# Kernel tuning notes

Measured on AMD Instinct MI355X. Metric: run time of the kernel, lower is better.

The kernel has to match this reference:

```python
import jax, jax.numpy as jnp
import numpy as np

N = 200000
HID = 256
HEADS = 8
HD = HID // HEADS
C = 1000  # num clusters


def setup_inputs() -> dict:
    key = jax.random.key(0)
    ks = jax.random.split(key, 8)
    s = 1.0 / np.sqrt(HID)
    return {
        "x": jax.random.normal(ks[0], (N, HID), dtype=jnp.float32),
        "cluster_assignments": jax.random.randint(ks[1], (N,), 0, C),
        "batch": jnp.zeros((N,), dtype=jnp.int64),
        "Wk": jax.random.uniform(ks[2], (HID, HID), minval=-s, maxval=s),
        "bk": jnp.zeros((HID,), dtype=jnp.float32),
        "Wv": jax.random.uniform(ks[3], (HID, HID), minval=-s, maxval=s),
        "bv": jnp.zeros((HID,), dtype=jnp.float32),
        "Wo": jax.random.uniform(ks[4], (HID, HID), minval=-s, maxval=s),
        "bo": jnp.zeros((HID,), dtype=jnp.float32),
        "pool_query": jax.random.normal(ks[5], (1, HEADS, HD), dtype=jnp.float32),
    }


def reference(x, cluster_assignments, batch, Wk, bk, Wv, bv, Wo, bo, pool_query):
    seg = cluster_assignments
    scale = HD ** -0.5
    keys = (x @ Wk.T + bk).reshape(-1, HEADS, HD)     # [N, H, D]
    values = (x @ Wv.T + bv).reshape(-1, HEADS, HD)   # [N, H, D]
    # attention scores per node/head against shared pool query
    scores = jnp.einsum('nhd,hd->nh', keys, pool_query[0]) * scale  # [N, H]
    # segment-wise (per-cluster) softmax over nodes, per head
    m = jax.ops.segment_max(scores, seg, num_segments=C)            # [C, H]
    e = jnp.exp(scores - m[seg])                                    # [N, H]
    z = jax.ops.segment_sum(e, seg, num_segments=C)                 # [C, H]
    w = e / z[seg]                                                  # [N, H]
    attended = (w[..., None] * values).reshape(-1, HID)             # [N, HID]
    # scatter_mean over clusters
    ssum = jax.ops.segment_sum(attended, seg, num_segments=C)       # [C, HID]
    cnt = jax.ops.segment_sum(jnp.ones((attended.shape[0],), attended.dtype), seg, num_segments=C)
    pooled = ssum / jnp.clip(cnt, 1.0)[:, None]                     # [C, HID]
    out = pooled @ Wo.T + bo                                        # [C, HID]
    return out[seg]                                                 # [N, HID]
```

## Files before the change

kernel.cpp:

```cpp
#include <hip/hip_runtime.h>
#include <math.h>

#define HID 256
#define HEADS 8
#define HD 32
#define C_CLUST 1000
#define SCALEQ 0.17677669529663687f
#define CAP 512

typedef float fx4 __attribute__((ext_vector_type(4)));

__global__ __launch_bounds__(256) void k_prep(const float* __restrict__ Wk,
                                              const float* __restrict__ bk,
                                              const float* __restrict__ pq,
                                              float* __restrict__ qk,
                                              float* __restrict__ cb,
                                              int* __restrict__ cur) {
  __shared__ float qv[HD];
  int h = blockIdx.x;
  int t = threadIdx.x;
  int g = h * 256 + t;
  for (int i = g; i < C_CLUST; i += 2048) cur[i] = 0;
  if (t < HD) qv[t] = pq[h * HD + t];
  __syncthreads();
  float a = 0.f;
#pragma unroll 8
  for (int d = 0; d < HD; ++d) a += Wk[(size_t)(h * HD + d) * HID + t] * qv[d];
  qk[h * HID + t] = a * SCALEQ;
  if (t == 0) {
    float s = 0.f;
    for (int d = 0; d < HD; ++d) s += bk[h * HD + d] * qv[d];
    cb[h] = s * SCALEQ;
  }
}

__global__ __launch_bounds__(256) void k_scores(const float* __restrict__ x,
                                                const int* __restrict__ seg,
                                                const float* __restrict__ qk,
                                                const float* __restrict__ cb,
                                                float* __restrict__ escr,
                                                int* __restrict__ cur,
                                                int* __restrict__ list, int N) {
  int lane = threadIdx.x & 63;
  int wid = (int)(((size_t)blockIdx.x * blockDim.x + threadIdx.x) >> 6);
  int nw = (int)(((size_t)gridDim.x * blockDim.x) >> 6);
  float4 q4[8];
#pragma unroll
  for (int h = 0; h < 8; ++h) q4[h] = *(const float4*)(qk + h * HID + 4 * lane);
  float cbv = cb[lane & 7];
  for (int n = wid; n < N; n += nw) {
    float4 xv = *(const float4*)(x + (size_t)n * HID + 4 * lane);
    float r0 = xv.x * q4[0].x + xv.y * q4[0].y + xv.z * q4[0].z + xv.w * q4[0].w;
    float r1 = xv.x * q4[1].x + xv.y * q4[1].y + xv.z * q4[1].z + xv.w * q4[1].w;
    float r2 = xv.x * q4[2].x + xv.y * q4[2].y + xv.z * q4[2].z + xv.w * q4[2].w;
    float r3 = xv.x * q4[3].x + xv.y * q4[3].y + xv.z * q4[3].z + xv.w * q4[3].w;
    float r4 = xv.x * q4[4].x + xv.y * q4[4].y + xv.z * q4[4].z + xv.w * q4[4].w;
    float r5 = xv.x * q4[5].x + xv.y * q4[5].y + xv.z * q4[5].z + xv.w * q4[5].w;
    float r6 = xv.x * q4[6].x + xv.y * q4[6].y + xv.z * q4[6].z + xv.w * q4[6].w;
    float r7 = xv.x * q4[7].x + xv.y * q4[7].y + xv.z * q4[7].z + xv.w * q4[7].w;
    r0 += __shfl_xor(r0, 1); r0 += __shfl_xor(r0, 2); r0 += __shfl_xor(r0, 4);
    r1 += __shfl_xor(r1, 1); r1 += __shfl_xor(r1, 2); r1 += __shfl_xor(r1, 4);
    r2 += __shfl_xor(r2, 1); r2 += __shfl_xor(r2, 2); r2 += __shfl_xor(r2, 4);
    r3 += __shfl_xor(r3, 1); r3 += __shfl_xor(r3, 2); r3 += __shfl_xor(r3, 4);
    r4 += __shfl_xor(r4, 1); r4 += __shfl_xor(r4, 2); r4 += __shfl_xor(r4, 4);
    r5 += __shfl_xor(r5, 1); r5 += __shfl_xor(r5, 2); r5 += __shfl_xor(r5, 4);
    r6 += __shfl_xor(r6, 1); r6 += __shfl_xor(r6, 2); r6 += __shfl_xor(r6, 4);
    r7 += __shfl_xor(r7, 1); r7 += __shfl_xor(r7, 2); r7 += __shfl_xor(r7, 4);
    int p = lane & 7;
    float v = (p < 4) ? ((p < 2) ? (p == 0 ? r0 : r1) : (p == 2 ? r2 : r3))
                      : ((p < 6) ? (p == 4 ? r4 : r5) : (p == 6 ? r6 : r7));
    v += __shfl_xor(v, 8); v += __shfl_xor(v, 16); v += __shfl_xor(v, 32);
    v += cbv;
    if (lane < 8) {
      int c = seg[n];
      escr[(size_t)n * 8 + lane] = __expf(v);
      if (lane == 0) {
        int pos = atomicAdd(&cur[c], 1);
        if (pos < CAP) list[c * CAP + pos] = n;
      }
    }
  }
}

__global__ __launch_bounds__(256) void k_pool(const float* __restrict__ x,
                                              const float* __restrict__ escr,
                                              const int* __restrict__ cur,
                                              const int* __restrict__ list,
                                              const float* __restrict__ Wv,
                                              const float* __restrict__ bv,
                                              const float* __restrict__ Wo,
                                              const float* __restrict__ bo,
                                              float* __restrict__ out) {
  __shared__ float e_lds[CAP][8];
  __shared__ float s_lds[8 * HID];
  __shared__ float red[32];
  __shared__ float p_lds[HID];
  __shared__ float orow[HID];
  int c = blockIdx.x;
  int t = threadIdx.x;
  int cnt = cur[c];
  if (cnt == 0) return;
  int cntL = (cnt < CAP) ? cnt : CAP;

  int h8 = t & 7;
  int i0 = t >> 3;
  int rq = t >> 6, cl = t & 63;
  const int* lp = list + c * CAP;

  float pz = 0.f;
  for (int i = i0; i < cntL; i += 32) {
    float ev = escr[(size_t)lp[i] * 8 + h8];
    e_lds[i][h8] = ev;
    pz += ev;
  }
  pz += __shfl_xor(pz, 8);
  pz += __shfl_xor(pz, 16);
  pz += __shfl_xor(pz, 32);
  if (cl < 8) red[rq * 8 + cl] = pz;
  __syncthreads();

  float4 acc[8];
#pragma unroll
  for (int h = 0; h < 8; ++h) acc[h] = make_float4(0.f, 0.f, 0.f, 0.f);
  const float* xb = x + 4 * cl;
#define ACC8(XV, ROW)                                                          \
  { float4 ea = *(const float4*)&e_lds[ROW][0];                                \
    float4 eb = *(const float4*)&e_lds[ROW][4];                                \
    float eh[8] = {ea.x, ea.y, ea.z, ea.w, eb.x, eb.y, eb.z, eb.w};            \
    _Pragma("unroll")                                                          \
    for (int h = 0; h < 8; ++h) {                                              \
      acc[h].x += eh[h] * XV.x; acc[h].y += eh[h] * XV.y;                      \
      acc[h].z += eh[h] * XV.z; acc[h].w += eh[h] * XV.w; } }
  int i = rq;
  for (; i + 28 < cntL; i += 32) {
    int n0 = lp[i +  0], n1 = lp[i +  4], n2 = lp[i +  8], n3 = lp[i + 12];
    int n4 = lp[i + 16], n5 = lp[i + 20], n6 = lp[i + 24], n7 = lp[i + 28];
    float4 x0 = *(const float4*)(xb + (size_t)n0 * HID);
    float4 x1 = *(const float4*)(xb + (size_t)n1 * HID);
    float4 x2 = *(const float4*)(xb + (size_t)n2 * HID);
    float4 x3 = *(const float4*)(xb + (size_t)n3 * HID);
    float4 x4 = *(const float4*)(xb + (size_t)n4 * HID);
    float4 x5 = *(const float4*)(xb + (size_t)n5 * HID);
    float4 x6 = *(const float4*)(xb + (size_t)n6 * HID);
    float4 x7 = *(const float4*)(xb + (size_t)n7 * HID);
    ACC8(x0, i +  0) ACC8(x1, i +  4) ACC8(x2, i +  8) ACC8(x3, i + 12)
    ACC8(x4, i + 16) ACC8(x5, i + 20) ACC8(x6, i + 24) ACC8(x7, i + 28)
  }
  for (; i < cntL; i += 4) {
    int n0 = lp[i];
    float4 x0 = *(const float4*)(xb + (size_t)n0 * HID);
    ACC8(x0, i)
  }
#undef ACC8

  float zinv[8];
#pragma unroll
  for (int h = 0; h < 8; ++h) {
    float z = red[h] + red[8 + h] + red[16 + h] + red[24 + h];
    zinv[h] = (z > 0.f) ? 1.f / z : 0.f;
  }

  float4* buf = (float4*)e_lds;
#pragma unroll
  for (int hp = 0; hp < 8; hp += 4) {
    __syncthreads();
#pragma unroll
    for (int h = 0; h < 4; ++h) buf[h * 256 + t] = acc[hp + h];
    __syncthreads();
    int hh = t >> 6;
    float4 a = buf[hh * 256 + cl];
    float4 b = buf[hh * 256 + cl + 64];
    float4 c4 = buf[hh * 256 + cl + 128];
    float4 d4 = buf[hh * 256 + cl + 192];
    float sc = zinv[hp + hh];
    float4 r;
    r.x = (a.x + b.x + c4.x + d4.x) * sc;
    r.y = (a.y + b.y + c4.y + d4.y) * sc;
    r.z = (a.z + b.z + c4.z + d4.z) * sc;
    r.w = (a.w + b.w + c4.w + d4.w) * sc;
    *(float4*)&s_lds[(hp + hh) * HID + 4 * cl] = r;
  }
  __syncthreads();

  int grp = t >> 2, q = t & 3;
  float rc = 1.f / (float)cnt;
#pragma unroll
  for (int r = 0; r < 4; ++r) {
    int o = grp + 64 * r;
    const float4* wr = (const float4*)(Wv + (size_t)o * HID);
    const float4* sr = (const float4*)(s_lds + (o >> 5) * HID);
    float a = 0.f;
#pragma unroll
    for (int k = 0; k < 16; ++k) {
      float4 w4 = wr[q + 4 * k];
      float4 s4 = sr[q + 4 * k];
      a += w4.x * s4.x + w4.y * s4.y + w4.z * s4.z + w4.w * s4.w;
    }
    a += __shfl_xor(a, 1);
    a += __shfl_xor(a, 2);
    if (q == 0) p_lds[o] = (a + bv[o]) * rc;
  }
  __syncthreads();
#pragma unroll
  for (int r = 0; r < 4; ++r) {
    int o = grp + 64 * r;
    const float4* wr = (const float4*)(Wo + (size_t)o * HID);
    const float4* pr = (const float4*)p_lds;
    float a = 0.f;
#pragma unroll
    for (int k = 0; k < 16; ++k) {
      float4 w4 = wr[q + 4 * k];
      float4 p4 = pr[q + 4 * k];
      a += w4.x * p4.x + w4.y * p4.y + w4.z * p4.z + w4.w * p4.w;
    }
    a += __shfl_xor(a, 1);
    a += __shfl_xor(a, 2);
    if (q == 0) orow[o] = a + bo[o];
  }
  __syncthreads();

  fx4 ov = *(const fx4*)&orow[4 * cl];
  for (int j = rq; j < cnt; j += 4) {
    int n = lp[j];
    __builtin_nontemporal_store(ov, (fx4*)(out + (size_t)n * HID + 4 * cl));
  }
}

extern "C" void kernel_launch(void* const* d_in, const int* in_sizes, int n_in,
                              void* d_out, int out_size, void* d_ws, size_t ws_size,
                              hipStream_t stream) {
  const float* x = (const float*)d_in[0];
  const int* seg = (const int*)d_in[1];
  const float* Wk = (const float*)d_in[3];
  const float* bk = (const float*)d_in[4];
  const float* Wv = (const float*)d_in[5];
  const float* bv = (const float*)d_in[6];
  const float* Wo = (const float*)d_in[7];
  const float* bo = (const float*)d_in[8];
  const float* pq = (const float*)d_in[9];
  int N = in_sizes[0] / HID;

  char* ws = (char*)d_ws;
  size_t cur_off = 0;
  auto take = [&](size_t bytes) -> void* {
    void* p = ws + cur_off;
    cur_off += (bytes + 255) & ~(size_t)255;
    return p;
  };
  float* qk = (float*)take((size_t)HEADS * HID * 4);
  float* cb = (float*)take((size_t)HEADS * 4);
  int* cur = (int*)take((size_t)C_CLUST * 4);
  int* list = (int*)take((size_t)C_CLUST * CAP * 4);
  float* scr = (float*)take((size_t)N * 8 * 4);

  k_prep<<<HEADS, 256, 0, stream>>>(Wk, bk, pq, qk, cb, cur);
  int sb = (N + 31) / 32;
  k_scores<<<sb, 256, 0, stream>>>(x, seg, qk, cb, scr, cur, list, N);
  k_pool<<<C_CLUST, 256, 0, stream>>>(x, scr, cur, list, Wv, bv, Wo, bo,
                                      (float*)d_out);
}
```

Before: 189.6 us.

## Fuse score computation into per-cluster pooling kernel with lightweight scatter pass

Replaces the streaming score kernel with a tiny scatter kernel that only builds per-cluster node lists. The per-node exp-scores are now computed inside the per-cluster pooling kernel, which grows to 512 threads (8 waves). This drops the score scratch buffer and avoids a separate full pass over x just for scores. In exchange each cluster block reads its x rows twice (once for scores, once for accumulation), which the cache may serve. The output store loop is now bounded by the capped count instead of the full count.

After: 237.3 us. 1.25x slower.

```diff
diff --git a/kernel.cpp b/kernel.cpp
--- a/kernel.cpp
+++ b/kernel.cpp
@@ -7,6 +7,7 @@
 #define C_CLUST 1000
 #define SCALEQ 0.17677669529663687f
 #define CAP 512
+#define NW 8
 
 typedef float fx4 __attribute__((ext_vector_type(4)));
 
@@ -34,22 +35,48 @@
   }
 }
 
-__global__ __launch_bounds__(256) void k_scores(const float* __restrict__ x,
-                                                const int* __restrict__ seg,
-                                                const float* __restrict__ qk,
-                                                const float* __restrict__ cb,
-                                                float* __restrict__ escr,
-                                                int* __restrict__ cur,
-                                                int* __restrict__ list, int N) {
-  int lane = threadIdx.x & 63;
-  int wid = (int)(((size_t)blockIdx.x * blockDim.x + threadIdx.x) >> 6);
-  int nw = (int)(((size_t)gridDim.x * blockDim.x) >> 6);
+__global__ __launch_bounds__(256) void k_scatter(const int* __restrict__ seg,
+                                                 int* __restrict__ cur,
+                                                 int* __restrict__ list, int N) {
+  int n = blockIdx.x * 256 + threadIdx.x;
+  if (n < N) {
+    int c = seg[n];
+    int pos = atomicAdd(&cur[c], 1);
+    if (pos < CAP) list[c * CAP + pos] = n;
+  }
+}
+
+__global__ __launch_bounds__(512) void k_fused(const float* __restrict__ x,
+                                               const int* __restrict__ cur,
+                                               const int* __restrict__ list,
+                                               const float* __restrict__ qk,
+                                               const float* __restrict__ cb,
+                                               const float* __restrict__ Wv,
+                                               const float* __restrict__ bv,
+                                               const float* __restrict__ Wo,
+                                               const float* __restrict__ bo,
+                                               float* __restrict__ out) {
+  __shared__ float e_lds[CAP][8];
+  __shared__ float s_lds[8 * HID];
+  __shared__ float red[NW * 8];
+  __shared__ float p_lds[HID];
+  __shared__ float orow[HID];
+  int c = blockIdx.x;
+  int t = threadIdx.x;
+  int cnt = cur[c];
+  if (cnt == 0) return;
+  int cntL = (cnt < CAP) ? cnt : CAP;
+  int w = t >> 6, l = t & 63;
+  const int* lp = list + c * CAP;
+
   float4 q4[8];
 #pragma unroll
-  for (int h = 0; h < 8; ++h) q4[h] = *(const float4*)(qk + h * HID + 4 * lane);
-  float cbv = cb[lane & 7];
-  for (int n = wid; n < N; n += nw) {
-    float4 xv = *(const float4*)(x + (size_t)n * HID + 4 * lane);
+  for (int h = 0; h < 8; ++h) q4[h] = *(const float4*)(qk + h * HID + 4 * l);
+  float cbv = cb[l & 7];
+  float zacc = 0.f;
+  for (int i = w; i < cntL; i += NW) {
+    int n = lp[i];
+    float4 xv = *(const float4*)(x + (size_t)n * HID + 4 * l);
     float r0 = xv.x * q4[0].x + xv.y * q4[0].y + xv.z * q4[0].z + xv.w * q4[0].w;
     float r1 = xv.x * q4[1].x + xv.y * q4[1].y + xv.z * q4[1].z + xv.w * q4[1].w;
     float r2 = xv.x * q4[2].x + xv.y * q4[2].y + xv.z * q4[2].z + xv.w * q4[2].w;
@@ -66,63 +93,22 @@
     r5 += __shfl_xor(r5, 1); r5 += __shfl_xor(r5, 2); r5 += __shfl_xor(r5, 4);
     r6 += __shfl_xor(r6, 1); r6 += __shfl_xor(r6, 2); r6 += __shfl_xor(r6, 4);
     r7 += __shfl_xor(r7, 1); r7 += __shfl_xor(r7, 2); r7 += __shfl_xor(r7, 4);
-    int p = lane & 7;
+    int p = l & 7;
     float v = (p < 4) ? ((p < 2) ? (p == 0 ? r0 : r1) : (p == 2 ? r2 : r3))
                       : ((p < 6) ? (p == 4 ? r4 : r5) : (p == 6 ? r6 : r7));
     v += __shfl_xor(v, 8); v += __shfl_xor(v, 16); v += __shfl_xor(v, 32);
     v += cbv;
-    if (lane < 8) {
-      int c = seg[n];
-      escr[(size_t)n * 8 + lane] = __expf(v);
-      if (lane == 0) {
-        int pos = atomicAdd(&cur[c], 1);
-        if (pos < CAP) list[c * CAP + pos] = n;
-      }
-    }
-  }
-}
-
-__global__ __launch_bounds__(256) void k_pool(const float* __restrict__ x,
-                                              const float* __restrict__ escr,
-                                              const int* __restrict__ cur,
-                                              const int* __restrict__ list,
-                                              const float* __restrict__ Wv,
-                                              const float* __restrict__ bv,
-                                              const float* __restrict__ Wo,
-                                              const float* __restrict__ bo,
-                                              float* __restrict__ out) {
-  __shared__ float e_lds[CAP][8];
-  __shared__ float s_lds[8 * HID];
-  __shared__ float red[32];
-  __shared__ float p_lds[HID];
-  __shared__ float orow[HID];
-  int c = blockIdx.x;
-  int t = threadIdx.x;
-  int cnt = cur[c];
-  if (cnt == 0) return;
-  int cntL = (cnt < CAP) ? cnt : CAP;
-
-  int h8 = t & 7;
-  int i0 = t >> 3;
-  int rq = t >> 6, cl = t & 63;
-  const int* lp = list + c * CAP;
-
-  float pz = 0.f;
-  for (int i = i0; i < cntL; i += 32) {
-    float ev = escr[(size_t)lp[i] * 8 + h8];
-    e_lds[i][h8] = ev;
-    pz += ev;
-  }
-  pz += __shfl_xor(pz, 8);
-  pz += __shfl_xor(pz, 16);
-  pz += __shfl_xor(pz, 32);
-  if (cl < 8) red[rq * 8 + cl] = pz;
+    float ev = __expf(v);
+    zacc += ev;
+    if (l < 8) e_lds[i][l] = ev;
+  }
+  if (l < 8) red[w * 8 + l] = zacc;
   __syncthreads();
 
   float4 acc[8];
 #pragma unroll
   for (int h = 0; h < 8; ++h) acc[h] = make_float4(0.f, 0.f, 0.f, 0.f);
-  const float* xb = x + 4 * cl;
+  const float* xb = x + 4 * l;
 #define ACC8(XV, ROW)                                                          \
   { float4 ea = *(const float4*)&e_lds[ROW][0];                                \
     float4 eb = *(const float4*)&e_lds[ROW][4];                                \
@@ -131,10 +117,10 @@
     for (int h = 0; h < 8; ++h) {                                              \
       acc[h].x += eh[h] * XV.x; acc[h].y += eh[h] * XV.y;                      \
       acc[h].z += eh[h] * XV.z; acc[h].w += eh[h] * XV.w; } }
-  int i = rq;
-  for (; i + 28 < cntL; i += 32) {
-    int n0 = lp[i +  0], n1 = lp[i +  4], n2 = lp[i +  8], n3 = lp[i + 12];
-    int n4 = lp[i + 16], n5 = lp[i + 20], n6 = lp[i + 24], n7 = lp[i + 28];
+  int i = w;
+  for (; i + 7 * NW < cntL; i += 8 * NW) {
+    int n0 = lp[i + 0 * NW], n1 = lp[i + 1 * NW], n2 = lp[i + 2 * NW], n3 = lp[i + 3 * NW];
+    int n4 = lp[i + 4 * NW], n5 = lp[i + 5 * NW], n6 = lp[i + 6 * NW], n7 = lp[i + 7 * NW];
     float4 x0 = *(const float4*)(xb + (size_t)n0 * HID);
     float4 x1 = *(const float4*)(xb + (size_t)n1 * HID);
     float4 x2 = *(const float4*)(xb + (size_t)n2 * HID);
@@ -143,10 +129,10 @@
     float4 x5 = *(const float4*)(xb + (size_t)n5 * HID);
     float4 x6 = *(const float4*)(xb + (size_t)n6 * HID);
     float4 x7 = *(const float4*)(xb + (size_t)n7 * HID);
-    ACC8(x0, i +  0) ACC8(x1, i +  4) ACC8(x2, i +  8) ACC8(x3, i + 12)
-    ACC8(x4, i + 16) ACC8(x5, i + 20) ACC8(x6, i + 24) ACC8(x7, i + 28)
-  }
-  for (; i < cntL; i += 4) {
+    ACC8(x0, i + 0 * NW) ACC8(x1, i + 1 * NW) ACC8(x2, i + 2 * NW) ACC8(x3, i + 3 * NW)
+    ACC8(x4, i + 4 * NW) ACC8(x5, i + 5 * NW) ACC8(x6, i + 6 * NW) ACC8(x7, i + 7 * NW)
+  }
+  for (; i < cntL; i += NW) {
     int n0 = lp[i];
     float4 x0 = *(const float4*)(xb + (size_t)n0 * HID);
     ACC8(x0, i)
@@ -156,37 +142,39 @@
   float zinv[8];
 #pragma unroll
   for (int h = 0; h < 8; ++h) {
-    float z = red[h] + red[8 + h] + red[16 + h] + red[24 + h];
+    float z = 0.f;
+#pragma unroll
+    for (int w2 = 0; w2 < NW; ++w2) z += red[w2 * 8 + h];
     zinv[h] = (z > 0.f) ? 1.f / z : 0.f;
   }
 
   float4* buf = (float4*)e_lds;
 #pragma unroll
-  for (int hp = 0; hp < 8; hp += 4) {
+  for (int hp = 0; hp < 8; hp += 2) {
     __syncthreads();
-#pragma unroll
-    for (int h = 0; h < 4; ++h) buf[h * 256 + t] = acc[hp + h];
+    buf[t] = acc[hp];
+    buf[512 + t] = acc[hp + 1];
     __syncthreads();
-    int hh = t >> 6;
-    float4 a = buf[hh * 256 + cl];
-    float4 b = buf[hh * 256 + cl + 64];
-    float4 c4 = buf[hh * 256 + cl + 128];
-    float4 d4 = buf[hh * 256 + cl + 192];
-    float sc = zinv[hp + hh];
-    float4 r;
-    r.x = (a.x + b.x + c4.x + d4.x) * sc;
-    r.y = (a.y + b.y + c4.y + d4.y) * sc;
-    r.z = (a.z + b.z + c4.z + d4.z) * sc;
-    r.w = (a.w + b.w + c4.w + d4.w) * sc;
-    *(float4*)&s_lds[(hp + hh) * HID + 4 * cl] = r;
+    if (t < 128) {
+      int hh = t >> 6, cl = t & 63;
+      float4 s = buf[hh * 512 + cl];
+#pragma unroll
+      for (int w2 = 1; w2 < NW; ++w2) {
+        float4 b = buf[hh * 512 + w2 * 64 + cl];
+        s.x += b.x; s.y += b.y; s.z += b.z; s.w += b.w;
+      }
+      float sc = zinv[hp + hh];
+      s.x *= sc; s.y *= sc; s.z *= sc; s.w *= sc;
+      *(float4*)&s_lds[(hp + hh) * HID + 4 * cl] = s;
+    }
   }
   __syncthreads();
 
   int grp = t >> 2, q = t & 3;
   float rc = 1.f / (float)cnt;
 #pragma unroll
-  for (int r = 0; r < 4; ++r) {
-    int o = grp + 64 * r;
+  for (int r = 0; r < 2; ++r) {
+    int o = grp + 128 * r;
     const float4* wr = (const float4*)(Wv + (size_t)o * HID);
     const float4* sr = (const float4*)(s_lds + (o >> 5) * HID);
     float a = 0.f;
@@ -202,8 +190,8 @@
   }
   __syncthreads();
 #pragma unroll
-  for (int r = 0; r < 4; ++r) {
-    int o = grp + 64 * r;
+  for (int r = 0; r < 2; ++r) {
+    int o = grp + 128 * r;
     const float4* wr = (const float4*)(Wo + (size_t)o * HID);
     const float4* pr = (const float4*)p_lds;
     float a = 0.f;
@@ -219,10 +207,10 @@
   }
   __syncthreads();
 
-  fx4 ov = *(const fx4*)&orow[4 * cl];
-  for (int j = rq; j < cnt; j += 4) {
+  fx4 ov = *(const fx4*)&orow[4 * l];
+  for (int j = w; j < cntL; j += NW) {
     int n = lp[j];
-    __builtin_nontemporal_store(ov, (fx4*)(out + (size_t)n * HID + 4 * cl));
+    __builtin_nontemporal_store(ov, (fx4*)(out + (size_t)n * HID + 4 * l));
   }
 }
 
@@ -251,11 +239,9 @@
   float* cb = (float*)take((size_t)HEADS * 4);
   int* cur = (int*)take((size_t)C_CLUST * 4);
   int* list = (int*)take((size_t)C_CLUST * CAP * 4);
-  float* scr = (float*)take((size_t)N * 8 * 4);
 
   k_prep<<<HEADS, 256, 0, stream>>>(Wk, bk, pq, qk, cb, cur);
-  int sb = (N + 31) / 32;
-  k_scores<<<sb, 256, 0, stream>>>(x, seg, qk, cb, scr, cur, list, N);
-  k_pool<<<C_CLUST, 256, 0, stream>>>(x, scr, cur, list, Wv, bv, Wo, bo,
-                                      (float*)d_out);
-}
+  k_scatter<<<(N + 255) / 256, 256, 0, stream>>>(seg, cur, list, N);
+  k_fused<<<C_CLUST, 512, 0, stream>>>(x, cur, list, qk, cb, Wv, bv, Wo, bo,
+                                       (float*)d_out);
+}
```
